# Optimization experiments

Measured on AMD Instinct MI355X. Metric: run time of the kernel, lower is better.

## Reference

```python
import jax, jax.numpy as jnp
import numpy as np

B, T, C, H, W = 2, 8, 256, 24, 24
NH = 8
HC = C // NH          # 32 head channels
KT, KHW = 3, 9        # offset conv kernel
ST, SHW = 2, 8        # offset conv stride
EPS = 1e-5


def _p(key, shape):
    return jax.random.normal(key, shape, dtype=jnp.float32) * 0.05


def setup_inputs() -> dict:
    ks = jax.random.split(jax.random.key(0), 16)
    return {
        "x": jax.random.normal(ks[0], (B, T, C, H, W), dtype=jnp.float32),
        "w_in": _p(ks[1], (C, C)), "b_in": _p(ks[2], (C,)),
        "w_q": _p(ks[3], (C, C)), "b_q": _p(ks[4], (C,)),
        "w_off_dw": _p(ks[5], (HC, 1, KT, KHW, KHW)), "b_off_dw": _p(ks[6], (HC,)),
        "ln_g": jnp.ones((HC,), jnp.float32), "ln_b": jnp.zeros((HC,), jnp.float32),
        "w_off_proj": _p(ks[7], (3, HC)),
        "w_k": _p(ks[8], (C, C)), "b_k": _p(ks[9], (C,)),
        "w_v": _p(ks[10], (C, C)), "b_v": _p(ks[11], (C,)),
        "rpe_w1": _p(ks[12], (32, 3)), "rpe_b1": _p(ks[13], (32,)),
        "rpe_w2": _p(ks[14], (1, 32)),
    }


def _conv1x1(x, w, b):
    # x: (B,C,T,H,W), w: (Co,Ci) -> pointwise Conv3d
    return jnp.einsum('bcthw,oc->bothw', x, w) + b[None, :, None, None, None]


def _trilinear(img, gx, gy, gz):
    # torch F.grid_sample(mode='bilinear', align_corners=True) for 5D input.
    # img: (G,Ch,T,H,W); gx->W axis, gy->H axis, gz->T axis, coords in [-1,1], shape (G,S)
    G, Ch, Td, Hd, Wd = img.shape
    ix = (gx + 1.0) * 0.5 * (Wd - 1)
    iy = (gy + 1.0) * 0.5 * (Hd - 1)
    iz = (gz + 1.0) * 0.5 * (Td - 1)
    x0 = jnp.floor(ix); y0 = jnp.floor(iy); z0 = jnp.floor(iz)
    fx = ix - x0; fy = iy - y0; fz = iz - z0
    x0i = jnp.clip(x0.astype(jnp.int32), 0, Wd - 1); x1i = jnp.clip(x0i + 1, 0, Wd - 1)
    y0i = jnp.clip(y0.astype(jnp.int32), 0, Hd - 1); y1i = jnp.clip(y0i + 1, 0, Hd - 1)
    z0i = jnp.clip(z0.astype(jnp.int32), 0, Td - 1); z1i = jnp.clip(z0i + 1, 0, Td - 1)
    bidx = jnp.arange(G)[:, None]

    def g(zi, yi, xi):
        return img[bidx, :, zi, yi, xi]  # (G,S,Ch)

    wz0, wz1 = (1.0 - fz)[..., None], fz[..., None]
    wy0, wy1 = (1.0 - fy)[..., None], fy[..., None]
    wx0, wx1 = (1.0 - fx)[..., None], fx[..., None]
    return (g(z0i, y0i, x0i) * wz0 * wy0 * wx0 + g(z0i, y0i, x1i) * wz0 * wy0 * wx1 +
            g(z0i, y1i, x0i) * wz0 * wy1 * wx0 + g(z0i, y1i, x1i) * wz0 * wy1 * wx1 +
            g(z1i, y0i, x0i) * wz1 * wy0 * wx0 + g(z1i, y0i, x1i) * wz1 * wy0 * wx1 +
            g(z1i, y1i, x0i) * wz1 * wy1 * wx0 + g(z1i, y1i, x1i) * wz1 * wy1 * wx1)


def reference(x, w_in, b_in, w_q, b_q, w_off_dw, b_off_dw, ln_g, ln_b, w_off_proj,
              w_k, b_k, w_v, b_v, rpe_w1, rpe_b1, rpe_w2):
    scale = HC ** (-0.5)
    xc = _conv1x1(jnp.transpose(x, (0, 2, 1, 3, 4)), w_in, b_in)       # (B,C,T,H,W)
    q = _conv1x1(xc, w_q, b_q)
    q_off = q.reshape(B * NH, HC, T, H, W)
    # depthwise offset conv: kernel (3,9,9), stride (2,8,8), pad (1,4,4)
    off = jax.lax.conv_general_dilated(
        q_off, w_off_dw, (ST, SHW, SHW),
        ((KT // 2, KT // 2), (KHW // 2, KHW // 2), (KHW // 2, KHW // 2)),
        dimension_numbers=('NCDHW', 'OIDHW', 'NCDHW'), feature_group_count=HC)
    off = off + b_off_dw[None, :, None, None, None]
    Tk, Hk, Wk = off.shape[2], off.shape[3], off.shape[4]
    o = jnp.transpose(off, (0, 2, 3, 4, 1))                             # (G,Tk,Hk,Wk,HC)
    mu = o.mean(-1, keepdims=True)
    var = ((o - mu) ** 2).mean(-1, keepdims=True)
    o = (o - mu) / jnp.sqrt(var + EPS) * ln_g + ln_b
    o = jax.nn.gelu(o, approximate=False)
    offset = jnp.einsum('bthwc,pc->bthwp', o, w_off_proj)               # (G,Tk,Hk,Wk,3)
    # reference points (linspace(0.5, K-0.5, K) normalized by (K-1))
    rt = ((jnp.arange(Tk, dtype=jnp.float32) + 0.5) / (Tk - 1.0)) * 2.0 - 1.0
    ry = ((jnp.arange(Hk, dtype=jnp.float32) + 0.5) / (Hk - 1.0)) * 2.0 - 1.0
    rx = ((jnp.arange(Wk, dtype=jnp.float32) + 0.5) / (Wk - 1.0)) * 2.0 - 1.0
    ref = jnp.stack(jnp.meshgrid(rt, ry, rx, indexing='ij'), axis=-1)   # (Tk,Hk,Wk,3)
    pos = jnp.clip(offset + ref, -1.0, 1.0)                             # offset_range_factor < 0 path
    G = B * NH
    n = Tk * Hk * Wk
    m = T * H * W
    posf = pos.reshape(G, n, 3)                                         # (t, y, x)
    # torch passes grid = pos[..., (0,2,1)] -> grid (x_w, y_h, z_t) = (pos_t, pos_x, pos_y)
    xs = _trilinear(xc.reshape(G, HC, T, H, W), posf[..., 0], posf[..., 2], posf[..., 1])  # (G,n,HC)
    x_sampled = jnp.transpose(xs, (0, 2, 1)).reshape(B, C, Tk, Hk, Wk)
    k = _conv1x1(x_sampled, w_k, b_k).reshape(G, HC, n)
    v = _conv1x1(x_sampled, w_v, b_v).reshape(G, HC, n)
    qf = q.reshape(G, HC, m)
    attn = jnp.einsum('bcm,bcn->bmn', qf, k) * scale                    # (G,m,n)
    # log-CPB bias (source normalizes y by W-1 and x by H-1; faithful)
    qt = (jnp.arange(T, dtype=jnp.float32) / (T - 1.0)) * 2.0 - 1.0
    qy = (jnp.arange(H, dtype=jnp.float32) / (W - 1.0)) * 2.0 - 1.0
    qx = (jnp.arange(W, dtype=jnp.float32) / (H - 1.0)) * 2.0 - 1.0
    qg = jnp.stack(jnp.meshgrid(qt, qy, qx, indexing='ij'), axis=-1).reshape(m, 3)
    disp = (qg[None, :, None, :] - posf[:, None, :, :]) * 4.0           # (G,m,n,3)
    disp = jnp.sign(disp) * jnp.log2(jnp.abs(disp) + 1.0) / 3.0         # log2(8) = 3
    hbias = jax.nn.relu(jnp.einsum('gmnp,hp->gmnh', disp, rpe_w1) + rpe_b1)
    attn = attn + jnp.einsum('gmnh,oh->gmno', hbias, rpe_w2)[..., 0]
    attn = jax.nn.softmax(attn, axis=2)
    out = jnp.einsum('bmn,bcn->bcm', attn, v).reshape(B, C, T, H, W)
    return jnp.transpose(out, (0, 2, 1, 3, 4))                          # (B,T,C,H,W)
```

## Files before the change

### kernel.cpp

```cpp
#include <hip/hip_runtime.h>
#include <hip/hip_bf16.h>

typedef unsigned short ushortT;
typedef __attribute__((ext_vector_type(8))) short bf16x8;
typedef __attribute__((ext_vector_type(4))) float f32x4;

#define WS_XC   0
#define WS_QB   2359296
#define WS_POS  3538944
#define WS_K    3540736
#define WS_V    3559168
#define WS_WC   3577600
#define WS_B512 3675904
#define WS_DTAB 3676416

__device__ __forceinline__ float bf2f(ushortT u) {
  union { unsigned int i; float f; } c; c.i = ((unsigned int)u) << 16; return c.f;
}
__device__ __forceinline__ ushortT f2bf(float f) {
  union { float f; unsigned int i; } c; c.f = f;
  unsigned int lsb = (c.i >> 16) & 1;
  return (ushortT)((c.i + 0x7fff + lsb) >> 16);
}
__device__ __forceinline__ float ldg_f(const void* p, int i, int bf) {
  return bf ? bf2f(((const ushortT*)p)[i]) : ((const float*)p)[i];
}
__device__ __forceinline__ int detect_bf(const void* x) {
  const ushortT* u = (const ushortT*)x;
  int wild = 0;
#pragma unroll
  for (int i = 0; i < 32; i++) {
    int e = (u[i] >> 7) & 0xFF;
    wild += (e != 0 && (e < 90 || e > 160)) ? 1 : 0;
  }
  return wild <= 4;
}
__device__ __forceinline__ float logmap(float d) {
  return copysignf(__log2f(fabsf(d) + 1.f) * (1.f / 3.f), d);
}

__global__ __launch_bounds__(256) void k_wc(const void* x, const void* w_in, const void* b_in,
                                            const void* w_q, const void* b_q,
                                            float* wc, float* bias512) {
  int o = blockIdx.x, tid = threadIdx.x;
  int bf = detect_bf(x);
  __shared__ float wq_s[256];
  __shared__ float red[256];
  wq_s[tid] = ldg_f(w_q, o * 256 + tid, bf);
  __syncthreads();
  float s = 0.f;
#pragma unroll 8
  for (int j = 0; j < 256; j++) s += wq_s[j] * ldg_f(w_in, j * 256 + tid, bf);
  wc[o * 256 + tid] = s;
  red[tid] = wq_s[tid] * ldg_f(b_in, tid, bf);
  __syncthreads();
  for (int m = 128; m; m >>= 1) {
    if (tid < m) red[tid] += red[tid + m];
    __syncthreads();
  }
  if (tid == 0) bias512[256 + o] = red[0] + ldg_f(b_q, o, bf);
  if (o == 0) bias512[tid] = ldg_f(b_in, tid, bf);
}

__global__ __launch_bounds__(256) void k_gemm_mfma(const void* x, const void* w_in, const float* wc,
                                                   const float* bias512, float* xc, ushortT* qb) {
  const int bf = detect_bf(x);
  __shared__ ushortT Ah[2][64 * 40], Al[2][64 * 40];
  __shared__ ushortT Bh[2][64 * 40], Bl[2][64 * 40];
  int tid = threadIdx.x;
  int bid = blockIdx.x;
  int colT = bid / 144, rowT = bid % 144;
  int col0 = colT * 64;
  int row0 = rowT * 64;
  int bt = row0 / 576;
  int hw0 = row0 % 576;
  const int isW = (col0 < 256);
  const ushortT* xB = (const ushortT*)x;
  const float*   xF = (const float*)x;
  const ushortT* wB = (const ushortT*)w_in;
  const float*   wF = (const float*)w_in;
  int ar = tid & 63, aoct = tid >> 6;
  int bn = tid >> 2, bko = tid & 3;
  int w = tid >> 6, l = tid & 63;
  int wr = w >> 1, wcq = w & 1;
  int lr = l & 15, lk = l >> 4;
  f32x4 acc[2][2] = {};

  float va[8], vb[8];
  auto loadA = [&](int kt) {
    int kbase = (bt * 256 + kt * 32 + aoct * 8) * 576 + hw0 + ar;
#pragma unroll
    for (int j = 0; j < 8; j++)
      va[j] = bf ? bf2f(xB[kbase + j * 576]) : xF[kbase + j * 576];
  };
  auto loadB = [&](int kt) {
    if (isW) {
      if (bf) {
        const ushortT* pp = wB + (col0 + bn) * 256 + kt * 32 + bko * 8;
#pragma unroll
        for (int j = 0; j < 8; j++) vb[j] = bf2f(pp[j]);
      } else {
        const float* pp = wF + (col0 + bn) * 256 + kt * 32 + bko * 8;
        float4 f0 = *(const float4*)pp;
        float4 f1 = *(const float4*)(pp + 4);
        vb[0] = f0.x; vb[1] = f0.y; vb[2] = f0.z; vb[3] = f0.w;
        vb[4] = f1.x; vb[5] = f1.y; vb[6] = f1.z; vb[7] = f1.w;
      }
    } else {
      const float* pp = wc + (col0 - 256 + bn) * 256 + kt * 32 + bko * 8;
      float4 f0 = *(const float4*)pp;
      float4 f1 = *(const float4*)(pp + 4);
      vb[0] = f0.x; vb[1] = f0.y; vb[2] = f0.z; vb[3] = f0.w;
      vb[4] = f1.x; vb[5] = f1.y; vb[6] = f1.z; vb[7] = f1.w;
    }
  };
  auto writeAB = [&](int buf) {
    unsigned ua[8], ra[8];
#pragma unroll
    for (int j = 0; j < 8; j++) {
      ua[j] = __float_as_uint(va[j]);
      ra[j] = __float_as_uint(va[j] - __uint_as_float(ua[j] & 0xffff0000u));
    }
    int4 ph, pl;
    ph.x = (int)((ua[0] >> 16) | (ua[1] & 0xffff0000u));
    ph.y = (int)((ua[2] >> 16) | (ua[3] & 0xffff0000u));
    ph.z = (int)((ua[4] >> 16) | (ua[5] & 0xffff0000u));
    ph.w = (int)((ua[6] >> 16) | (ua[7] & 0xffff0000u));
    pl.x = (int)((ra[0] >> 16) | (ra[1] & 0xffff0000u));
    pl.y = (int)((ra[2] >> 16) | (ra[3] & 0xffff0000u));
    pl.z = (int)((ra[4] >> 16) | (ra[5] & 0xffff0000u));
    pl.w = (int)((ra[6] >> 16) | (ra[7] & 0xffff0000u));
    *(int4*)&Ah[buf][ar * 40 + aoct * 8] = ph;
    *(int4*)&Al[buf][ar * 40 + aoct * 8] = pl;
#pragma unroll
    for (int j = 0; j < 8; j++) {
      ua[j] = __float_as_uint(vb[j]);
      ra[j] = __float_as_uint(vb[j] - __uint_as_float(ua[j] & 0xffff0000u));
    }
    ph.x = (int)((ua[0] >> 16) | (ua[1] & 0xffff0000u));
    ph.y = (int)((ua[2] >> 16) | (ua[3] & 0xffff0000u));
    ph.z = (int)((ua[4] >> 16) | (ua[5] & 0xffff0000u));
    ph.w = (int)((ua[6] >> 16) | (ua[7] & 0xffff0000u));
    pl.x = (int)((ra[0] >> 16) | (ra[1] & 0xffff0000u));
    pl.y = (int)((ra[2] >> 16) | (ra[3] & 0xffff0000u));
    pl.z = (int)((ra[4] >> 16) | (ra[5] & 0xffff0000u));
    pl.w = (int)((ra[6] >> 16) | (ra[7] & 0xffff0000u));
    *(int4*)&Bh[buf][bn * 40 + bko * 8] = ph;
    *(int4*)&Bl[buf][bn * 40 + bko * 8] = pl;
  };

  loadA(0); loadB(0);
  writeAB(0);
  __syncthreads();
  for (int kt = 0; kt < 8; kt++) {
    int cur = kt & 1;
    if (kt < 7) { loadA(kt + 1); loadB(kt + 1); }
    bf16x8 a0h = *(const bf16x8*)&Ah[cur][(wr * 32 + 0 * 16 + lr) * 40 + lk * 8];
    bf16x8 a1h = *(const bf16x8*)&Ah[cur][(wr * 32 + 1 * 16 + lr) * 40 + lk * 8];
    bf16x8 a0l = *(const bf16x8*)&Al[cur][(wr * 32 + 0 * 16 + lr) * 40 + lk * 8];
    bf16x8 a1l = *(const bf16x8*)&Al[cur][(wr * 32 + 1 * 16 + lr) * 40 + lk * 8];
    bf16x8 b0h = *(const bf16x8*)&Bh[cur][(wcq * 32 + 0 * 16 + lr) * 40 + lk * 8];
    bf16x8 b1h = *(const bf16x8*)&Bh[cur][(wcq * 32 + 1 * 16 + lr) * 40 + lk * 8];
    bf16x8 b0l = *(const bf16x8*)&Bl[cur][(wcq * 32 + 0 * 16 + lr) * 40 + lk * 8];
    bf16x8 b1l = *(const bf16x8*)&Bl[cur][(wcq * 32 + 1 * 16 + lr) * 40 + lk * 8];
    acc[0][0] = __builtin_amdgcn_mfma_f32_16x16x32_bf16(a0h, b0h, acc[0][0], 0, 0, 0);
    acc[0][0] = __builtin_amdgcn_mfma_f32_16x16x32_bf16(a0h, b0l, acc[0][0], 0, 0, 0);
    acc[0][0] = __builtin_amdgcn_mfma_f32_16x16x32_bf16(a0l, b0h, acc[0][0], 0, 0, 0);
    acc[0][1] = __builtin_amdgcn_mfma_f32_16x16x32_bf16(a0h, b1h, acc[0][1], 0, 0, 0);
    acc[0][1] = __builtin_amdgcn_mfma_f32_16x16x32_bf16(a0h, b1l, acc[0][1], 0, 0, 0);
    acc[0][1] = __builtin_amdgcn_mfma_f32_16x16x32_bf16(a0l, b1h, acc[0][1], 0, 0, 0);
    acc[1][0] = __builtin_amdgcn_mfma_f32_16x16x32_bf16(a1h, b0h, acc[1][0], 0, 0, 0);
    acc[1][0] = __builtin_amdgcn_mfma_f32_16x16x32_bf16(a1h, b0l, acc[1][0], 0, 0, 0);
    acc[1][0] = __builtin_amdgcn_mfma_f32_16x16x32_bf16(a1l, b0h, acc[1][0], 0, 0, 0);
    acc[1][1] = __builtin_amdgcn_mfma_f32_16x16x32_bf16(a1h, b1h, acc[1][1], 0, 0, 0);
    acc[1][1] = __builtin_amdgcn_mfma_f32_16x16x32_bf16(a1h, b1l, acc[1][1], 0, 0, 0);
    acc[1][1] = __builtin_amdgcn_mfma_f32_16x16x32_bf16(a1l, b1h, acc[1][1], 0, 0, 0);
    if (kt < 7) writeAB(cur ^ 1);
    __syncthreads();
  }
#pragma unroll
  for (int m = 0; m < 2; m++) {
#pragma unroll
    for (int n = 0; n < 2; n++) {
#pragma unroll
      for (int i = 0; i < 4; i++) {
        int row = row0 + wr * 32 + m * 16 + lk * 4 + i;
        int col = col0 + wcq * 32 + n * 16 + lr;
        float v = acc[m][n][i] + bias512[col];
        if (isW) xc[row * 256 + col] = v;
        else     qb[row * 256 + (col - 256)] = f2bf(v);
      }
    }
  }
}

__global__ __launch_bounds__(256) void k_offsets(const void* x, const ushortT* qb, const void* w_dw,
                                                 const void* b_dw, const void* ln_g, const void* ln_b,
                                                 const void* w_proj, float* pos, float* dtab) {
  __shared__ float wdw[243 * 33];
  __shared__ float part[8][33];
  __shared__ float ptile[3];
  int bid = blockIdx.x;
  int g = bid / 36, nn = bid % 36;
  int b = g >> 3, nh = g & 7;
  int tk = nn / 9, hk = (nn / 3) % 3, wk = nn % 3;
  int tid = threadIdx.x;
  int ch = tid & 31, grp = tid >> 5;
  int bf = detect_bf(x);
  for (int i = tid; i < 7776; i += 256) {
    int c = i / 243, tap = i % 243;
    wdw[tap * 33 + c] = ldg_f(w_dw, i, bf);
  }
  __syncthreads();
  float sum = 0.f;
  for (int tap = grp; tap < 243; tap += 8) {
    int dt = tap / 81, rem = tap % 81, dh = rem / 9, dw = rem % 9;
    int t = tk * 2 - 1 + dt, h = hk * 8 - 4 + dh, w = wk * 8 - 4 + dw;
    if (t < 0 || t >= 8 || h < 0 || h >= 24 || w < 0 || w >= 24) continue;
    float qv = bf2f(qb[((b * 8 + t) * 576 + h * 24 + w) * 256 + nh * 32 + ch]);
    sum += qv * wdw[tap * 33 + ch];
  }
  part[grp][ch] = sum;
  __syncthreads();
  if (tid < 32) {
    float v = ldg_f(b_dw, ch, bf);
#pragma unroll
    for (int j = 0; j < 8; j++) v += part[j][ch];
    float s1 = v;
    for (int m = 16; m; m >>= 1) s1 += __shfl_xor(s1, m);
    float mu = s1 * (1.f / 32.f);
    float d = v - mu;
    float s2 = d * d;
    for (int m = 16; m; m >>= 1) s2 += __shfl_xor(s2, m);
    float o = d * rsqrtf(s2 * (1.f / 32.f) + 1e-5f) * ldg_f(ln_g, ch, bf) + ldg_f(ln_b, ch, bf);
    o = 0.5f * o * (1.f + erff(o * 0.70710678118654752f));
    float res[3];
#pragma unroll
    for (int p = 0; p < 3; p++) {
      float t3 = o * ldg_f(w_proj, p * 32 + ch, bf);
      for (int m = 16; m; m >>= 1) t3 += __shfl_xor(t3, m);
      res[p] = t3;
    }
    if (ch == 0) {
      float ref0 = ((tk + 0.5f) / 3.f) * 2.f - 1.f;
      float ref1 = ((hk + 0.5f) / 2.f) * 2.f - 1.f;
      float ref2 = ((wk + 0.5f) / 2.f) * 2.f - 1.f;
      float p0 = fminf(1.f, fmaxf(-1.f, res[0] + ref0));
      float p1 = fminf(1.f, fmaxf(-1.f, res[1] + ref1));
      float p2 = fminf(1.f, fmaxf(-1.f, res[2] + ref2));
      pos[bid * 3 + 0] = p0;
      pos[bid * 3 + 1] = p1;
      pos[bid * 3 + 2] = p2;
      ptile[0] = p0; ptile[1] = p1; ptile[2] = p2;
    }
  }
  __syncthreads();
  if (tid < 56) {
    float dv;
    if (tid < 8)       dv = ((float)tid       * (2.f / 7.f)  - 1.f - ptile[0]) * 4.f;
    else if (tid < 32) dv = ((float)(tid - 8) * (2.f / 23.f) - 1.f - ptile[1]) * 4.f;
    else               dv = ((float)(tid - 32)* (2.f / 23.f) - 1.f - ptile[2]) * 4.f;
    dtab[bid * 56 + tid] = logmap(dv);
  }
}

__global__ __launch_bounds__(256) void k_svkv(const void* x, const float* xc_rm, const float* pos,
                                              const void* w_k, const void* b_k,
                                              const void* w_v, const void* b_v,
                                              float* k_rm, float* v_rm) {
  int bx = blockIdx.x;
  int row = bx >> 2, quad = bx & 3;
  int sel = quad >> 1, colhalf = quad & 1;
  int b = row / 36, nn = row % 36;
  int tid = threadIdx.x;
  int bf = detect_bf(x);
  __shared__ float a[256];
  {
    int nh = tid >> 5;
    int g = b * 8 + nh;
    float p0 = pos[(g * 36 + nn) * 3 + 0];
    float p1 = pos[(g * 36 + nn) * 3 + 1];
    float p2 = pos[(g * 36 + nn) * 3 + 2];
    float ix = (p0 + 1.f) * 0.5f * 23.f;
    float iy = (p2 + 1.f) * 0.5f * 23.f;
    float iz = (p1 + 1.f) * 0.5f * 7.f;
    float x0f = floorf(ix), y0f = floorf(iy), z0f = floorf(iz);
    float fx = ix - x0f, fy = iy - y0f, fz = iz - z0f;
    int x0 = min(max((int)x0f, 0), 23), x1 = min(x0 + 1, 23);
    int y0 = min(max((int)y0f, 0), 23), y1 = min(y0 + 1, 23);
    int z0 = min(max((int)z0f, 0), 7),  z1 = min(z0 + 1, 7);
#define AT(z, y, x) xc_rm[(((b * 8 + (z)) * 576 + (y) * 24 + (x)) * 256 + tid)]
    a[tid] =
      AT(z0, y0, x0) * (1.f - fz) * (1.f - fy) * (1.f - fx) + AT(z0, y0, x1) * (1.f - fz) * (1.f - fy) * fx +
      AT(z0, y1, x0) * (1.f - fz) * fy * (1.f - fx)         + AT(z0, y1, x1) * (1.f - fz) * fy * fx +
      AT(z1, y0, x0) * fz * (1.f - fy) * (1.f - fx)         + AT(z1, y0, x1) * fz * (1.f - fy) * fx +
      AT(z1, y1, x0) * fz * fy * (1.f - fx)                 + AT(z1, y1, x1) * fz * fy * fx;
#undef AT
  }
  __syncthreads();
  const void* w = sel ? w_v : w_k;
  const void* bb = sel ? b_v : b_k;
  int col = colhalf * 128 + (tid >> 1);
  int half = tid & 1;
  int c0 = half * 128;
  float s = 0.f;
  if (bf) {
    const ushortT* wp = (const ushortT*)w + col * 256 + c0;
#pragma unroll 4
    for (int c = 0; c < 128; c += 8) {
      ushort4 k0 = *(const ushort4*)(wp + c), k1 = *(const ushort4*)(wp + c + 4);
      s += a[c0+c+0]*bf2f(k0.x) + a[c0+c+1]*bf2f(k0.y) + a[c0+c+2]*bf2f(k0.z) + a[c0+c+3]*bf2f(k0.w)
         + a[c0+c+4]*bf2f(k1.x) + a[c0+c+5]*bf2f(k1.y) + a[c0+c+6]*bf2f(k1.z) + a[c0+c+7]*bf2f(k1.w);
    }
  } else {
    const float* wp = (const float*)w + col * 256 + c0;
#pragma unroll 8
    for (int c = 0; c < 128; c += 4) {
      float4 k4 = *(const float4*)(wp + c);
      s += a[c0+c]*k4.x + a[c0+c+1]*k4.y + a[c0+c+2]*k4.z + a[c0+c+3]*k4.w;
    }
  }
  s += __shfl_xor(s, 1);
  if (half == 0) {
    float* outp = sel ? v_rm : k_rm;
    outp[row * 256 + col] = s + ldg_f(bb, col, bf);
  }
}

__global__ __launch_bounds__(256) void k_attn(const void* x, const ushortT* qb,
                                              const float* k_rm, const float* v_rm,
                                              const float* dtab, const void* rpe_w1,
                                              const void* rpe_b1, const void* rpe_w2, void* outp) {
  __shared__ float ks[36][32];
  __shared__ float vs[36][32];
  __shared__ float dt[36][57];
  int g = blockIdx.y, b = g >> 3, nh = g & 7;
  int tid = threadIdx.x;
  int bf = detect_bf(x);
  for (int e = tid; e < 36 * 32; e += 256) {
    int nn = e >> 5, ch = e & 31;
    ks[nn][ch] = k_rm[(b * 36 + nn) * 256 + nh * 32 + ch];
    vs[nn][ch] = v_rm[(b * 36 + nn) * 256 + nh * 32 + ch];
  }
  for (int e = tid; e < 36 * 56; e += 256) dt[e / 56][e % 56] = dtab[g * 2016 + e];
  __syncthreads();

  int sub = tid & 7, chb = sub * 4;
  int mm = blockIdx.x * 32 + (tid >> 3);
  int t = mm / 576, hw = mm % 576, hh = hw / 24, wwi = hw % 24;
  float qreg[4];
  {
    ushort4 u = *(const ushort4*)&qb[(b * 4608 + mm) * 256 + nh * 32 + chb];
    qreg[0] = bf2f(u.x); qreg[1] = bf2f(u.y); qreg[2] = bf2f(u.z); qreg[3] = bf2f(u.w);
  }
  float wx[4], wy[4], wz[4], wb_[4], w2[4];
#pragma unroll
  for (int j = 0; j < 4; j++) {
    int h = chb + j;
    wx[j]  = ldg_f(rpe_w1, h * 3 + 0, bf);
    wy[j]  = ldg_f(rpe_w1, h * 3 + 1, bf);
    wz[j]  = ldg_f(rpe_w1, h * 3 + 2, bf);
    wb_[j] = ldg_f(rpe_b1, h, bf);
    w2[j]  = ldg_f(rpe_w2, h, bf);
  }
  const float scale = 0.17677669529663687f;
  float p[36];
#pragma unroll
  for (int nn = 0; nn < 36; nn++) {
    float s = 0.f;
#pragma unroll
    for (int j = 0; j < 4; j++) s += qreg[j] * ks[nn][chb + j];
    s *= scale;
    float d0 = dt[nn][t];
    float d1 = dt[nn][8 + hh];
    float d2 = dt[nn][32 + wwi];
#pragma unroll
    for (int j = 0; j < 4; j++) {
      float hb = fmaf(d0, wx[j], fmaf(d1, wy[j], fmaf(d2, wz[j], wb_[j])));
      s = fmaf(fmaxf(hb, 0.f), w2[j], s);
    }
    p[nn] = s;
  }
#pragma unroll
  for (int nn = 0; nn < 36; nn++) {
    p[nn] += __shfl_xor(p[nn], 1);
    p[nn] += __shfl_xor(p[nn], 2);
    p[nn] += __shfl_xor(p[nn], 4);
  }
  float mx = -1e30f;
#pragma unroll
  for (int nn = 0; nn < 36; nn++) mx = fmaxf(mx, p[nn]);
  float se = 0.f;
#pragma unroll
  for (int nn = 0; nn < 36; nn++) {
    float e = __expf(p[nn] - mx);
    p[nn] = e;
    se += e;
  }
  float inv = 1.f / se;
  float acc[4] = {};
#pragma unroll
  for (int nn = 0; nn < 36; nn++) {
    float pr = p[nn] * inv;
#pragma unroll
    for (int j = 0; j < 4; j++) acc[j] += pr * vs[nn][chb + j];
  }
  int obase = ((b * 8 + t) * 256 + nh * 32 + chb) * 576 + hw;
  if (bf) {
    __hip_bfloat16* o = (__hip_bfloat16*)outp;
#pragma unroll
    for (int j = 0; j < 4; j++) o[obase + j * 576] = __float2bfloat16(acc[j]);
  } else {
    float* o = (float*)outp;
#pragma unroll
    for (int j = 0; j < 4; j++) o[obase + j * 576] = acc[j];
  }
}

extern "C" void kernel_launch(void* const* d_in, const int* in_sizes, int n_in,
                              void* d_out, int out_size, void* d_ws, size_t ws_size,
                              hipStream_t stream) {
  const void* x        = d_in[0];
  const void* w_in     = d_in[1];
  const void* b_in     = d_in[2];
  const void* w_q      = d_in[3];
  const void* b_q      = d_in[4];
  const void* w_off_dw = d_in[5];
  const void* b_off_dw = d_in[6];
  const void* ln_g     = d_in[7];
  const void* ln_b     = d_in[8];
  const void* w_off_pj = d_in[9];
  const void* w_k      = d_in[10];
  const void* b_k      = d_in[11];
  const void* w_v      = d_in[12];
  const void* b_v      = d_in[13];
  const void* rpe_w1   = d_in[14];
  const void* rpe_b1   = d_in[15];
  const void* rpe_w2   = d_in[16];

  float* ws    = (float*)d_ws;
  float* xc    = ws + WS_XC;
  ushortT* qb  = (ushortT*)(ws + WS_QB);
  float* pos   = ws + WS_POS;
  float* krm   = ws + WS_K;
  float* vrm   = ws + WS_V;
  float* wcf   = ws + WS_WC;
  float* b512  = ws + WS_B512;
  float* dtab  = ws + WS_DTAB;

  k_wc<<<256, 256, 0, stream>>>(x, w_in, b_in, w_q, b_q, wcf, b512);
  k_gemm_mfma<<<1152, 256, 0, stream>>>(x, w_in, wcf, b512, xc, qb);
  k_offsets<<<576, 256, 0, stream>>>(x, qb, w_off_dw, b_off_dw, ln_g, ln_b, w_off_pj, pos, dtab);
  k_svkv<<<288, 256, 0, stream>>>(x, xc, pos, w_k, b_k, w_v, b_v, krm, vrm);
  k_attn<<<dim3(144, 16), 256, 0, stream>>>(x, qb, krm, vrm, dtab, rpe_w1, rpe_b1, rpe_w2, d_out);
}
```

Baseline: 117.8 us.

## Precompute RPE bias table in offsets kernel with packed fp16 math; bf16 K/V smem

Moves the relative-position-bias MLP out of the attention kernel into the offsets kernel. There it is computed once per (group, key, query) using packed fp16 FMAs and dot2 instructions, and written as a full fp32 bias table of about 2.6M floats. The attention kernel then only reads one bias value per key, and it keeps K/V in shared memory as bf16. This removes the MLP that the old code recomputed redundantly across 8 lanes, at the cost of a large extra global write and read and reduced precision in the bias and K/V values.

```diff
diff --git a/kernel.cpp b/kernel.cpp
--- a/kernel.cpp
+++ b/kernel.cpp
@@ -4,6 +4,7 @@
 typedef unsigned short ushortT;
 typedef __attribute__((ext_vector_type(8))) short bf16x8;
 typedef __attribute__((ext_vector_type(4))) float f32x4;
+typedef __fp16 half2v __attribute__((ext_vector_type(2)));
 
 #define WS_XC   0
 #define WS_QB   2359296
@@ -12,7 +13,7 @@
 #define WS_V    3559168
 #define WS_WC   3577600
 #define WS_B512 3675904
-#define WS_DTAB 3676416
+#define WS_BIAS 3676416
 
 __device__ __forceinline__ float bf2f(ushortT u) {
   union { unsigned int i; float f; } c; c.i = ((unsigned int)u) << 16; return c.f;
@@ -196,10 +197,13 @@
 
 __global__ __launch_bounds__(256) void k_offsets(const void* x, const ushortT* qb, const void* w_dw,
                                                  const void* b_dw, const void* ln_g, const void* ln_b,
-                                                 const void* w_proj, float* pos, float* dtab) {
+                                                 const void* w_proj, const void* rpe_w1,
+                                                 const void* rpe_b1, const void* rpe_w2,
+                                                 float* pos, float* biastab) {
   __shared__ float wdw[243 * 33];
   __shared__ float part[8][33];
   __shared__ float ptile[3];
+  __shared__ float dts[56];
   int bid = blockIdx.x;
   int g = bid / 36, nn = bid % 36;
   int b = g >> 3, nh = g & 7;
@@ -257,10 +261,38 @@
   __syncthreads();
   if (tid < 56) {
     float dv;
-    if (tid < 8)       dv = ((float)tid       * (2.f / 7.f)  - 1.f - ptile[0]) * 4.f;
-    else if (tid < 32) dv = ((float)(tid - 8) * (2.f / 23.f) - 1.f - ptile[1]) * 4.f;
-    else               dv = ((float)(tid - 32)* (2.f / 23.f) - 1.f - ptile[2]) * 4.f;
-    dtab[bid * 56 + tid] = logmap(dv);
+    if (tid < 8)       dv = ((float)tid        * (2.f / 7.f)  - 1.f - ptile[0]) * 4.f;
+    else if (tid < 32) dv = ((float)(tid - 8)  * (2.f / 23.f) - 1.f - ptile[1]) * 4.f;
+    else               dv = ((float)(tid - 32) * (2.f / 23.f) - 1.f - ptile[2]) * 4.f;
+    dts[tid] = logmap(dv);
+  }
+  __syncthreads();
+  half2v wxp[16], wyp[16], wzp[16], wbp[16], w2p[16];
+#pragma unroll
+  for (int j = 0; j < 16; j++) {
+    wxp[j] = __builtin_amdgcn_cvt_pkrtz(ldg_f(rpe_w1, (2*j)*3+0, bf), ldg_f(rpe_w1, (2*j+1)*3+0, bf));
+    wyp[j] = __builtin_amdgcn_cvt_pkrtz(ldg_f(rpe_w1, (2*j)*3+1, bf), ldg_f(rpe_w1, (2*j+1)*3+1, bf));
+    wzp[j] = __builtin_amdgcn_cvt_pkrtz(ldg_f(rpe_w1, (2*j)*3+2, bf), ldg_f(rpe_w1, (2*j+1)*3+2, bf));
+    wbp[j] = __builtin_amdgcn_cvt_pkrtz(ldg_f(rpe_b1, 2*j, bf), ldg_f(rpe_b1, 2*j+1, bf));
+    w2p[j] = __builtin_amdgcn_cvt_pkrtz(ldg_f(rpe_w2, 2*j, bf), ldg_f(rpe_w2, 2*j+1, bf));
+  }
+  half2v zero = __builtin_amdgcn_cvt_pkrtz(0.f, 0.f);
+  float* brow = biastab + bid * 4608;
+  for (int mm = tid; mm < 4608; mm += 256) {
+    int t = mm / 576, hw = mm % 576, hh = hw / 24, ww = hw % 24;
+    float d0 = dts[t], d1 = dts[8 + hh], d2 = dts[32 + ww];
+    half2v d0h = __builtin_amdgcn_cvt_pkrtz(d0, d0);
+    half2v d1h = __builtin_amdgcn_cvt_pkrtz(d1, d1);
+    half2v d2h = __builtin_amdgcn_cvt_pkrtz(d2, d2);
+    float s = 0.f;
+#pragma unroll
+    for (int j = 0; j < 16; j++) {
+      half2v hb = d0h * wxp[j] + (d1h * wyp[j] + (d2h * wzp[j] + wbp[j]));
+      half2v r;
+      asm("v_pk_max_f16 %0, %1, %2" : "=v"(r) : "v"(hb), "v"(zero));
+      asm("v_dot2_f32_f16 %0, %1, %2, %0" : "+v"(s) : "v"(r), "v"(w2p[j]));
+    }
+    brow[mm] = s;
   }
 }
 
@@ -329,63 +361,43 @@
 
 __global__ __launch_bounds__(256) void k_attn(const void* x, const ushortT* qb,
                                               const float* k_rm, const float* v_rm,
-                                              const float* dtab, const void* rpe_w1,
-                                              const void* rpe_b1, const void* rpe_w2, void* outp) {
-  __shared__ float ks[36][32];
-  __shared__ float vs[36][32];
-  __shared__ float dt[36][57];
+                                              const float* biastab, void* outp) {
+  __shared__ ushortT ksb[36][32];
+  __shared__ ushortT vsb[36][32];
   int g = blockIdx.y, b = g >> 3, nh = g & 7;
   int tid = threadIdx.x;
   int bf = detect_bf(x);
   for (int e = tid; e < 36 * 32; e += 256) {
     int nn = e >> 5, ch = e & 31;
-    ks[nn][ch] = k_rm[(b * 36 + nn) * 256 + nh * 32 + ch];
-    vs[nn][ch] = v_rm[(b * 36 + nn) * 256 + nh * 32 + ch];
-  }
-  for (int e = tid; e < 36 * 56; e += 256) dt[e / 56][e % 56] = dtab[g * 2016 + e];
+    ksb[nn][ch] = f2bf(k_rm[(b * 36 + nn) * 256 + nh * 32 + ch]);
+    vsb[nn][ch] = f2bf(v_rm[(b * 36 + nn) * 256 + nh * 32 + ch]);
+  }
   __syncthreads();
 
   int sub = tid & 7, chb = sub * 4;
   int mm = blockIdx.x * 32 + (tid >> 3);
-  int t = mm / 576, hw = mm % 576, hh = hw / 24, wwi = hw % 24;
+  int t = mm / 576, hw = mm % 576;
   float qreg[4];
   {
     ushort4 u = *(const ushort4*)&qb[(b * 4608 + mm) * 256 + nh * 32 + chb];
     qreg[0] = bf2f(u.x); qreg[1] = bf2f(u.y); qreg[2] = bf2f(u.z); qreg[3] = bf2f(u.w);
   }
-  float wx[4], wy[4], wz[4], wb_[4], w2[4];
-#pragma unroll
-  for (int j = 0; j < 4; j++) {
-    int h = chb + j;
-    wx[j]  = ldg_f(rpe_w1, h * 3 + 0, bf);
-    wy[j]  = ldg_f(rpe_w1, h * 3 + 1, bf);
-    wz[j]  = ldg_f(rpe_w1, h * 3 + 2, bf);
-    wb_[j] = ldg_f(rpe_b1, h, bf);
-    w2[j]  = ldg_f(rpe_w2, h, bf);
-  }
   const float scale = 0.17677669529663687f;
+  const float* brow = biastab + g * 36 * 4608 + mm;
   float p[36];
 #pragma unroll
   for (int nn = 0; nn < 36; nn++) {
-    float s = 0.f;
-#pragma unroll
-    for (int j = 0; j < 4; j++) s += qreg[j] * ks[nn][chb + j];
-    s *= scale;
-    float d0 = dt[nn][t];
-    float d1 = dt[nn][8 + hh];
-    float d2 = dt[nn][32 + wwi];
-#pragma unroll
-    for (int j = 0; j < 4; j++) {
-      float hb = fmaf(d0, wx[j], fmaf(d1, wy[j], fmaf(d2, wz[j], wb_[j])));
-      s = fmaf(fmaxf(hb, 0.f), w2[j], s);
-    }
-    p[nn] = s;
+    ushort4 k4 = *(const ushort4*)&ksb[nn][chb];
+    float s = qreg[0] * bf2f(k4.x) + qreg[1] * bf2f(k4.y)
+            + qreg[2] * bf2f(k4.z) + qreg[3] * bf2f(k4.w);
+    p[nn] = s * scale;
   }
 #pragma unroll
   for (int nn = 0; nn < 36; nn++) {
     p[nn] += __shfl_xor(p[nn], 1);
     p[nn] += __shfl_xor(p[nn], 2);
     p[nn] += __shfl_xor(p[nn], 4);
+    p[nn] += brow[nn * 4608];
   }
   float mx = -1e30f;
 #pragma unroll
@@ -402,8 +414,9 @@
 #pragma unroll
   for (int nn = 0; nn < 36; nn++) {
     float pr = p[nn] * inv;
-#pragma unroll
-    for (int j = 0; j < 4; j++) acc[j] += pr * vs[nn][chb + j];
+    ushort4 v4 = *(const ushort4*)&vsb[nn][chb];
+    acc[0] += pr * bf2f(v4.x); acc[1] += pr * bf2f(v4.y);
+    acc[2] += pr * bf2f(v4.z); acc[3] += pr * bf2f(v4.w);
   }
   int obase = ((b * 8 + t) * 256 + nh * 32 + chb) * 576 + hw;
   if (bf) {
@@ -438,19 +451,20 @@
   const void* rpe_b1   = d_in[15];
   const void* rpe_w2   = d_in[16];
 
-  float* ws    = (float*)d_ws;
-  float* xc    = ws + WS_XC;
-  ushortT* qb  = (ushortT*)(ws + WS_QB);
-  float* pos   = ws + WS_POS;
-  float* krm   = ws + WS_K;
-  float* vrm   = ws + WS_V;
-  float* wcf   = ws + WS_WC;
-  float* b512  = ws + WS_B512;
-  float* dtab  = ws + WS_DTAB;
+  float* ws     = (float*)d_ws;
+  float* xc     = ws + WS_XC;
+  ushortT* qb   = (ushortT*)(ws + WS_QB);
+  float* pos    = ws + WS_POS;
+  float* krm    = ws + WS_K;
+  float* vrm    = ws + WS_V;
+  float* wcf    = ws + WS_WC;
+  float* b512   = ws + WS_B512;
+  float* biastab = ws + WS_BIAS;
 
   k_wc<<<256, 256, 0, stream>>>(x, w_in, b_in, w_q, b_q, wcf, b512);
   k_gemm_mfma<<<1152, 256, 0, stream>>>(x, w_in, wcf, b512, xc, qb);
-  k_offsets<<<576, 256, 0, stream>>>(x, qb, w_off_dw, b_off_dw, ln_g, ln_b, w_off_pj, pos, dtab);
+  k_offsets<<<576, 256, 0, stream>>>(x, qb, w_off_dw, b_off_dw, ln_g, ln_b, w_off_pj,
+                                     rpe_w1, rpe_b1, rpe_w2, pos, biastab);
   k_svkv<<<288, 256, 0, stream>>>(x, xc, pos, w_k, b_k, w_v, b_v, krm, vrm);
-  k_attn<<<dim3(144, 16), 256, 0, stream>>>(x, qb, krm, vrm, dtab, rpe_w1, rpe_b1, rpe_w2, d_out);
-}
+  k_attn<<<dim3(144, 16), 256, 0, stream>>>(x, qb, krm, vrm, biastab, d_out);
+}
```

After: 124.1 us. 5.3% more time.
